# Kernel tuning notes

Measured on AMD Instinct MI355X. Metric: run time of the kernel, lower is better.

## Reference

```python
import jax, jax.numpy as jnp
import numpy as np

B, S, J, D = 8, 512, 25, 64      # batch, seq_len, n_joints, d_model
H, DH = 8, 32                    # n_heads, d_head
IN, OUT = J * D, J * DH * H      # 1600, 6400


def setup_inputs() -> dict:
    key = jax.random.key(0)
    ks = jax.random.split(key, 5)
    sc_in = 1.0 / np.sqrt(IN)
    sc_hd = 1.0 / np.sqrt(DH * H)
    return {
        "x": jax.random.normal(ks[0], (B, S, J, D), dtype=jnp.float32),
        # weights stored [in, out] (transpose of torch Linear.weight)
        "Wq": jax.random.normal(ks[1], (IN, OUT), dtype=jnp.float32) * sc_in,
        "Wk": jax.random.normal(ks[2], (IN, OUT), dtype=jnp.float32) * sc_in,
        "Wv": jax.random.normal(ks[3], (IN, OUT), dtype=jnp.float32) * sc_in,
        "Wb": jax.random.normal(ks[4], (DH * H, D), dtype=jnp.float32) * sc_hd,
    }


def reference(x, Wq, Wk, Wv, Wb):
    b, s, j, d = x.shape
    xf = x.reshape(b, s, j * d)                      # [B,S,J*D]
    q = xf @ Wq                                      # [B,S,OUT]
    k = xf @ Wk
    v = xf @ Wv
    # single fused attention over the full J*d_head*H width, scaled by d_model
    scores = jnp.einsum("bse,bte->bst", q, k) * (d ** -0.5)  # [B,S,S]
    causal = jnp.triu(jnp.ones((s, s), dtype=bool), k=1)
    scores = jnp.where(causal[None], -jnp.inf, scores)
    attn = jax.nn.softmax(scores, axis=-1)           # [B,S,S]
    ctx = jnp.einsum("bst,bte->bse", attn, v)        # [B,S,OUT]
    ctx = ctx.reshape(b, s, j, DH * H)               # [B,S,J,dh*H]
    out = ctx @ Wb                                   # [B,S,J,D]  (dropout = eval identity)
    return out
```

## Files before the change

### kernel.cpp

```cpp
#include <hip/hip_runtime.h>

typedef float  f32x4  __attribute__((ext_vector_type(4)));
typedef __bf16 bf16x8 __attribute__((ext_vector_type(8)));
typedef __bf16 bf16x4 __attribute__((ext_vector_type(4)));

__device__ __forceinline__ void gl_lds16(const void* g, void* l) {
    __builtin_amdgcn_global_load_lds(
        (const __attribute__((address_space(1))) void*)g,
        (__attribute__((address_space(3))) void*)l, 16, 0, 0);
}

__device__ __forceinline__ int xcd_swz(int wg, int nwg) {
    int xcd = wg & 7, idx = wg >> 3;
    int q = nwg >> 3, r = nwg & 7;
    return (xcd < r ? xcd * (q + 1) : r * (q + 1) + (xcd - r) * q) + idx;
}

__global__ void split_f32(const float* __restrict__ in, __bf16* __restrict__ hi,
                          __bf16* __restrict__ lo, long n) {
    long i = ((long)blockIdx.x * blockDim.x + threadIdx.x) * 4;
    if (i >= n) return;
    float4 v = *(const float4*)&in[i];
    bf16x4 h, l;
    h[0] = (__bf16)v.x; l[0] = (__bf16)(v.x - (float)h[0]);
    h[1] = (__bf16)v.y; l[1] = (__bf16)(v.y - (float)h[1]);
    h[2] = (__bf16)v.z; l[2] = (__bf16)(v.z - (float)h[2]);
    h[3] = (__bf16)v.w; l[3] = (__bf16)(v.w - (float)h[3]);
    *(bf16x4*)&hi[i] = h;
    *(bf16x4*)&lo[i] = l;
}

__global__ void copy_f32(const float* __restrict__ in, float* __restrict__ out) {
    long i = ((long)blockIdx.x * blockDim.x + threadIdx.x) * 4;
    *(float4*)&out[i] = *(const float4*)&in[i];
}

__global__ void cvt_wb(const float* __restrict__ Wb, __bf16* __restrict__ Wbt) {
    int idx = blockIdx.x * 256 + threadIdx.x;
    int k = idx >> 6, n = idx & 63;
    Wbt[n * 256 + k] = (__bf16)Wb[idx];
}

__global__ __launch_bounds__(256) void wvb_kernel(const float* __restrict__ Wv,
                                                  const __bf16* __restrict__ Wbt,
                                                  __bf16* __restrict__ WvbT) {
    const int kb = blockIdx.x;
    const int j  = blockIdx.y;
    const int tid = threadIdx.x;
    const int w = tid >> 6, l = tid & 63;
    const long r0 = (long)kb * 64 + w * 16;
    const int lr = l & 15, lk8 = (l >> 4) * 8;
    f32x4 acc[4];
    #pragma unroll
    for (int n = 0; n < 4; ++n) acc[n] = (f32x4){0.f, 0.f, 0.f, 0.f};
    #pragma unroll
    for (int kt = 0; kt < 8; ++kt) {
        const int k = kt * 32 + lk8;
        const float* ap = &Wv[(r0 + lr) * 6400 + j * 256 + k];
        float4 f0 = *(const float4*)ap;
        float4 f1 = *(const float4*)(ap + 4);
        bf16x8 a = {(__bf16)f0.x, (__bf16)f0.y, (__bf16)f0.z, (__bf16)f0.w,
                    (__bf16)f1.x, (__bf16)f1.y, (__bf16)f1.z, (__bf16)f1.w};
        #pragma unroll
        for (int n = 0; n < 4; ++n) {
            bf16x8 b = *(const bf16x8*)&Wbt[(n * 16 + lr) * 256 + k];
            acc[n] = __builtin_amdgcn_mfma_f32_16x16x32_bf16(a, b, acc[n], 0, 0, 0);
        }
    }
    const int rr = (l >> 4) * 4;
    #pragma unroll
    for (int n = 0; n < 4; ++n)
        #pragma unroll
        for (int r = 0; r < 4; ++r)
            WvbT[(long)(j * 64 + n * 16 + lr) * 1600 + r0 + rr + r] = (__bf16)acc[n][r];
}

template <int OUTMODE, bool CAUSAL, bool SWZ>
__global__ __launch_bounds__(256) void gemm3f(
    const __bf16* __restrict__ Ahi, const __bf16* __restrict__ Alo,
    const __bf16* __restrict__ Bhi, const __bf16* __restrict__ Blo,
    float* __restrict__ C, __bf16* __restrict__ Ch, __bf16* __restrict__ Cl,
    int ktot, int nkc, int lda, int ldb, int ldc, int M, int N,
    long sA, long sB, long sC, float scale)
{
    __shared__ __bf16 AsH[8192], AsL[8192], BsH[8192], BsL[8192];
    int bx = blockIdx.x, by = blockIdx.y;
    if (SWZ) {
        int f = xcd_swz(by * gridDim.x + bx, gridDim.x * gridDim.y);
        bx = f % gridDim.x; by = f / gridDim.x;
    }
    const int n0 = bx * 128, m0 = by * 128;
    if (CAUSAL && n0 > m0) return;
    const int bz = blockIdx.z;
    const int batch = bz / nkc, kc = bz % nkc;
    Ahi += (long)batch * sA; Alo += (long)batch * sA;
    Bhi += (long)batch * sB; Blo += (long)batch * sB;
    const int kbeg = (kc * ktot) / nkc;
    const int kend = ((kc + 1) * ktot) / nkc;

    const int tid = threadIdx.x;
    const int w = tid >> 6, l = tid & 63;
    const int wr = w >> 1, wc = w & 1;
    const int lr = l & 15;
    const int lk8 = (l >> 4) * 8;
    const int kswz = (lr & 7) << 3;
    const int srow = l >> 3;
    const int scol = ((l & 7) ^ (l >> 3)) * 8;

    f32x4 acc[4][4];
    #pragma unroll
    for (int m = 0; m < 4; ++m)
        #pragma unroll
        for (int n = 0; n < 4; ++n) acc[m][n] = (f32x4){0.f, 0.f, 0.f, 0.f};

    for (int kt = kbeg; kt < kend; ++kt) {
        const int k0 = kt << 6;
        __syncthreads();
        #pragma unroll
        for (int it = 0; it < 4; ++it) {
            const int j = it * 4 + w;
            const int grow = j * 8 + srow;
            const long ga = (long)(m0 + grow) * lda + k0 + scol;
            const long gb = (long)(n0 + grow) * ldb + k0 + scol;
            gl_lds16(Ahi + ga, &AsH[j * 512]);
            gl_lds16(Alo + ga, &AsL[j * 512]);
            gl_lds16(Bhi + gb, &BsH[j * 512]);
            gl_lds16(Blo + gb, &BsL[j * 512]);
        }
        __syncthreads();
        #pragma unroll
        for (int kk = 0; kk < 2; ++kk) {
            const int kx = (kk * 32 + lk8) ^ kswz;
            bf16x8 ah[4], bh[4], tt[4];
            #pragma unroll
            for (int m = 0; m < 4; ++m)
                ah[m] = *(const bf16x8*)&AsH[(wr * 64 + m * 16 + lr) * 64 + kx];
            #pragma unroll
            for (int n = 0; n < 4; ++n)
                bh[n] = *(const bf16x8*)&BsH[(wc * 64 + n * 16 + lr) * 64 + kx];
            #pragma unroll
            for (int m = 0; m < 4; ++m)
                #pragma unroll
                for (int n = 0; n < 4; ++n)
                    acc[m][n] = __builtin_amdgcn_mfma_f32_16x16x32_bf16(ah[m], bh[n], acc[m][n], 0, 0, 0);
            #pragma unroll
            for (int n = 0; n < 4; ++n)
                tt[n] = *(const bf16x8*)&BsL[(wc * 64 + n * 16 + lr) * 64 + kx];
            #pragma unroll
            for (int m = 0; m < 4; ++m)
                #pragma unroll
                for (int n = 0; n < 4; ++n)
                    acc[m][n] = __builtin_amdgcn_mfma_f32_16x16x32_bf16(ah[m], tt[n], acc[m][n], 0, 0, 0);
            #pragma unroll
            for (int m = 0; m < 4; ++m)
                tt[m] = *(const bf16x8*)&AsL[(wr * 64 + m * 16 + lr) * 64 + kx];
            #pragma unroll
            for (int m = 0; m < 4; ++m)
                #pragma unroll
                for (int n = 0; n < 4; ++n)
                    acc[m][n] = __builtin_amdgcn_mfma_f32_16x16x32_bf16(tt[m], bh[n], acc[m][n], 0, 0, 0);
        }
    }

    const int r0 = wr * 64 + (l >> 4) * 4;
    const int c0 = wc * 64 + lr;
    #pragma unroll
    for (int m = 0; m < 4; ++m)
        #pragma unroll
        for (int n = 0; n < 4; ++n)
            #pragma unroll
            for (int r = 0; r < 4; ++r) {
                int row = m0 + r0 + m * 16 + r;
                int col = n0 + c0 + n * 16;
                if (row < M && col < N) {
                    float v = acc[m][n][r] * scale;
                    long idx = (long)batch * sC + (long)row * ldc + col;
                    if (OUTMODE == 1) {
                        unsafeAtomicAdd(&C[idx], v);
                    } else if (OUTMODE == 2) {
                        __bf16 h = (__bf16)v;
                        Ch[idx] = h;
                        Cl[idx] = (__bf16)(v - (float)h);
                    } else {
                        C[idx] = v;
                    }
                }
            }
}

template <typename CT, bool TRANSC, bool SWZ>
__global__ __launch_bounds__(256) void gemm_bt(const __bf16* __restrict__ A,
                                               const __bf16* __restrict__ Bt,
                                               CT* __restrict__ C,
                                               int K, int lda, int ldb, int ldc,
                                               long sA, long sB, long sC,
                                               float scale, int causal, int Nlim) {
    __shared__ __bf16 As[8192];
    __shared__ __bf16 Bs[8192];
    int bx = blockIdx.x, by = blockIdx.y;
    if (SWZ) {
        int f = xcd_swz(by * gridDim.x + bx, gridDim.x * gridDim.y);
        bx = f % gridDim.x; by = f / gridDim.x;
    }
    const int n0 = bx * 128, m0 = by * 128;
    A  += (long)blockIdx.z * sA;
    Bt += (long)blockIdx.z * sB;
    int ksteps = K >> 6;
    if (causal == 2) { int lim = (m0 >> 6) + 2; if (lim < ksteps) ksteps = lim; }

    const int tid = threadIdx.x;
    const int w = tid >> 6, l = tid & 63;
    const int wr = w >> 1, wc = w & 1;
    const int lr = l & 15;
    const int lk8 = (l >> 4) * 8;
    const int kswz = (lr & 7) << 3;
    const int srow = l >> 3;
    const int scol = ((l & 7) ^ (l >> 3)) * 8;

    f32x4 acc[4][4];
    #pragma unroll
    for (int m = 0; m < 4; ++m)
        #pragma unroll
        for (int n = 0; n < 4; ++n) acc[m][n] = (f32x4){0.f, 0.f, 0.f, 0.f};

    for (int kt = 0; kt < ksteps; ++kt) {
        const int k0 = kt << 6;
        __syncthreads();
        #pragma unroll
        for (int it = 0; it < 4; ++it) {
            const int j = it * 4 + w;
            const int grow = j * 8 + srow;
            gl_lds16(A  + (long)(m0 + grow) * lda + k0 + scol, &As[j * 512]);
            gl_lds16(Bt + (long)(n0 + grow) * ldb + k0 + scol, &Bs[j * 512]);
        }
        __syncthreads();
        #pragma unroll
        for (int kk = 0; kk < 2; ++kk) {
            const int kx = (kk * 32 + lk8) ^ kswz;
            bf16x8 a[4], b[4];
            #pragma unroll
            for (int m = 0; m < 4; ++m)
                a[m] = *(const bf16x8*)&As[(wr * 64 + m * 16 + lr) * 64 + kx];
            #pragma unroll
            for (int n = 0; n < 4; ++n)
                b[n] = *(const bf16x8*)&Bs[(wc * 64 + n * 16 + lr) * 64 + kx];
            #pragma unroll
            for (int m = 0; m < 4; ++m)
                #pragma unroll
                for (int n = 0; n < 4; ++n)
                    acc[m][n] = __builtin_amdgcn_mfma_f32_16x16x32_bf16(a[m], b[n], acc[m][n], 0, 0, 0);
        }
    }

    const int r0 = m0 + wr * 64 + (l >> 4) * 4;
    const int c0 = n0 + wc * 64 + lr;
    #pragma unroll
    for (int m = 0; m < 4; ++m)
        #pragma unroll
        for (int n = 0; n < 4; ++n)
            #pragma unroll
            for (int r = 0; r < 4; ++r) {
                float v = acc[m][n][r] * scale;
                int row = r0 + m * 16 + r;
                int col = c0 + n * 16;
                if (TRANSC) {
                    C[(long)(row >> 9) * sC + (long)col * ldc + (row & 511)] = (CT)v;
                } else if (col < Nlim) {
                    C[(long)blockIdx.z * sC + (long)row * ldc + col] = (CT)v;
                }
            }
}

__global__ __launch_bounds__(256) void softmax_causal(const float* __restrict__ S,
                                                      __bf16* __restrict__ P) {
    __shared__ float red[8];
    const long rid = blockIdx.x;
    const int s = (int)(rid & 511);
    const float* row = S + rid * 512;
    __bf16* prow = P + rid * 512;
    const int t = threadIdx.x;
    float x0 = (t       <= s) ? row[t]       : -3.0e38f;
    float x1 = (t + 256 <= s) ? row[t + 256] : -3.0e38f;
    float m = fmaxf(x0, x1);
    #pragma unroll
    for (int off = 1; off < 64; off <<= 1) m = fmaxf(m, __shfl_xor(m, off));
    const int w = t >> 6;
    if ((t & 63) == 0) red[w] = m;
    __syncthreads();
    m = fmaxf(fmaxf(red[0], red[1]), fmaxf(red[2], red[3]));
    float e0 = __expf(x0 - m), e1 = __expf(x1 - m);
    float sum = e0 + e1;
    #pragma unroll
    for (int off = 1; off < 64; off <<= 1) sum += __shfl_xor(sum, off);
    if ((t & 63) == 0) red[4 + w] = sum;
    __syncthreads();
    sum = red[4] + red[5] + red[6] + red[7];
    const float rinv = 1.0f / sum;
    prow[t]       = (__bf16)(e0 * rinv);
    prow[t + 256] = (__bf16)(e1 * rinv);
}

extern "C" void kernel_launch(void* const* d_in, const int* in_sizes, int n_in,
                              void* d_out, int out_size, void* d_ws, size_t ws_size,
                              hipStream_t stream) {
    (void)in_sizes; (void)n_in; (void)out_size; (void)ws_size;
    const float* x  = (const float*)d_in[0];
    const float* Wq = (const float*)d_in[1];
    const float* Wk = (const float*)d_in[2];
    const float* Wv = (const float*)d_in[3];
    const float* Wb = (const float*)d_in[4];
    float* out = (float*)d_out;
    char* ws = (char*)d_ws;

    __bf16* Wqh = (__bf16*)(ws + 0);
    __bf16* Wql = (__bf16*)(ws + 20480000);
    __bf16* Wkh = (__bf16*)(ws + 40960000);
    __bf16* Wkl = (__bf16*)(ws + 61440000);
    float*  Gt  = (float*) (ws + 81920000);
    __bf16* Gth = (__bf16*)(ws + 92160000);
    __bf16* Gtl = (__bf16*)(ws + 97484800);
    __bf16* Wbt = (__bf16*)(ws + 102809600);
    __bf16* xh  = (__bf16*)(ws + 0);
    __bf16* xl  = (__bf16*)(ws + 13107200);
    __bf16* th  = (__bf16*)(ws + 26214400);
    __bf16* tl  = (__bf16*)(ws + 39321600);
    float*  s   = (float*) (ws + 81920000);
    __bf16* P   = (__bf16*)(ws + 90308608);
    __bf16* WvbT = (__bf16*)(ws + 39321600);
    __bf16* VWt  = (__bf16*)(ws + 44646400);
    float*  CtxF = (float*) (ws + 0);

    split_f32<<<10000, 256, 0, stream>>>(Wq, Wqh, Wql, 10240000L);
    split_f32<<<10000, 256, 0, stream>>>(Wk, Wkh, Wkl, 10240000L);
    hipMemsetAsync(Gt, 0, 10240000, stream);
    gemm3f<1, false, true><<<dim3(13, 13, 3), 256, 0, stream>>>(
        Wkh, Wkl, Wqh, Wql, Gt, nullptr, nullptr,
        100, 3, 6400, 6400, 1600, 1600, 1600, 0L, 0L, 0L, 1.0f);
    hipMemsetAsync((char*)Gth + 5120000, 0, 204800, stream);
    hipMemsetAsync((char*)Gtl + 5120000, 0, 204800, stream);
    split_f32<<<2500, 256, 0, stream>>>(Gt, Gth, Gtl, 2560000L);

    split_f32<<<6400, 256, 0, stream>>>(x, xh, xl, 6553600L);
    gemm3f<2, false, true><<<dim3(13, 32, 1), 256, 0, stream>>>(
        xh, xl, Gth, Gtl, nullptr, th, tl,
        25, 1, 1600, 1600, 1600, 4096, 1600, 0L, 0L, 0L, 1.0f);

    hipMemsetAsync(s, 0, 8388608, stream);
    gemm3f<1, true, false><<<dim3(4, 4, 40), 256, 0, stream>>>(
        th, tl, xh, xl, s, nullptr, nullptr,
        25, 5, 1600, 1600, 512, 512, 512, 819200L, 819200L, 262144L, 0.125f);

    softmax_causal<<<4096, 256, 0, stream>>>(s, P);

    cvt_wb<<<64, 256, 0, stream>>>(Wb, Wbt);
    hipMemsetAsync(WvbT, 0, 5324800, stream);
    wvb_kernel<<<dim3(25, 25), 256, 0, stream>>>(Wv, Wbt, WvbT);

    gemm_bt<__bf16, true, true><<<dim3(13, 32), 256, 0, stream>>>(
        xh, WvbT, VWt, 1600, 1600, 1600, 512, 0L, 0L, 851968L, 1.0f, 0, 1664);

    gemm_bt<float, false, false><<<dim3(13, 4, 8), 256, 0, stream>>>(
        P, VWt, CtxF, 512, 512, 512, 1600,
        262144L, 851968L, 819200L, 1.0f, 2, 1600);

    copy_f32<<<6400, 256, 0, stream>>>(CtxF, out);
}
```

Before: 355.4 us.

## Add 256x256-tile split-bf16 GEMM kernel for Gram and projection GEMMs

Adds gemm3v, a 512-thread kernel computing 256x256 output tiles with double-buffered LDS loads via global_load_lds. It walks the three hi/lo bf16 product terms as one flattened k-loop instead of separate passes. The Wk·Wq Gram GEMM and the x·G projection now use it with split-K atomics. The projection writes fp32 into a zeroed buffer and then runs an extra split pass into hi/lo bf16. This trades higher reuse per tile and fewer blocks for extra memset, atomic and split traffic, and edge tiles are partly wasted on the 1600-wide dimension.

```diff
diff --git a/kernel.cpp b/kernel.cpp
--- a/kernel.cpp
+++ b/kernel.cpp
@@ -73,6 +73,108 @@
         #pragma unroll
         for (int r = 0; r < 4; ++r)
             WvbT[(long)(j * 64 + n * 16 + lr) * 1600 + r0 + rr + r] = (__bf16)acc[n][r];
+}
+
+template <int OUTMODE, bool SWZ>
+__global__ __launch_bounds__(512, 2) void gemm3v(
+    const __bf16* __restrict__ Ahi, const __bf16* __restrict__ Alo,
+    const __bf16* __restrict__ Bhi, const __bf16* __restrict__ Blo,
+    float* __restrict__ C,
+    int ktot, int nkc, int lda, int ldb, int ldc, int M, int N, float scale)
+{
+    __shared__ __bf16 lds[2 * 32768];
+    int bx = blockIdx.x, by = blockIdx.y;
+    if (SWZ) {
+        int f = xcd_swz(by * gridDim.x + bx, gridDim.x * gridDim.y);
+        bx = f % gridDim.x; by = f / gridDim.x;
+    }
+    const int n0 = bx * 256, m0 = by * 256;
+    const int kc = blockIdx.z;
+    const int kbeg = (kc * ktot) / nkc;
+    const int L = ((kc + 1) * ktot) / nkc - kbeg;
+    const int KV = 3 * L;
+
+    const int tid = threadIdx.x;
+    const int w = tid >> 6, l = tid & 63;
+    const int wm = w >> 2, wn = w & 3;
+    const int lr = l & 15;
+    const int lk8 = (l >> 4) * 8;
+    const int kswz = (lr & 7) << 3;
+    const int srow = l >> 3;
+    const int scol = ((l & 7) ^ (l >> 3)) * 8;
+
+    f32x4 acc[8][4];
+    #pragma unroll
+    for (int mf = 0; mf < 8; ++mf)
+        #pragma unroll
+        for (int nf = 0; nf < 4; ++nf) acc[mf][nf] = (f32x4){0.f, 0.f, 0.f, 0.f};
+
+    auto STAGE = [&](int kv, int b) {
+        const int seg = (kv >= L) + (kv >= 2 * L);
+        const __bf16* As_ = (seg < 2) ? Ahi : Alo;
+        const __bf16* Bs_ = (seg == 1) ? Blo : Bhi;
+        const int k0 = (kbeg + kv - seg * L) << 6;
+        __bf16* base = lds + b * 32768;
+        #pragma unroll
+        for (int it = 0; it < 4; ++it) {
+            const int j = it * 8 + w;
+            const int grow = j * 8 + srow;
+            gl_lds16(As_ + (long)(m0 + grow) * lda + k0 + scol, base + j * 512);
+            gl_lds16(Bs_ + (long)(n0 + grow) * ldb + k0 + scol, base + 16384 + j * 512);
+        }
+    };
+
+    STAGE(0, 0);
+    for (int kv = 0; kv < KV; ++kv) {
+        const int cur = kv & 1;
+        if (kv + 1 < KV) {
+            STAGE(kv + 1, cur ^ 1);
+            asm volatile("s_waitcnt vmcnt(8)" ::: "memory");
+        } else {
+            asm volatile("s_waitcnt vmcnt(0)" ::: "memory");
+        }
+        __builtin_amdgcn_sched_barrier(0);
+        __builtin_amdgcn_s_barrier();
+        const __bf16* At = lds + cur * 32768;
+        const __bf16* Bt = At + 16384;
+        __builtin_amdgcn_s_setprio(1);
+        #pragma unroll
+        for (int kk = 0; kk < 2; ++kk) {
+            const int kx = (kk * 32 + lk8) ^ kswz;
+            bf16x8 a[8], b[4];
+            #pragma unroll
+            for (int mf = 0; mf < 8; ++mf)
+                a[mf] = *(const bf16x8*)&At[(wm * 128 + mf * 16 + lr) * 64 + kx];
+            #pragma unroll
+            for (int nf = 0; nf < 4; ++nf)
+                b[nf] = *(const bf16x8*)&Bt[(wn * 64 + nf * 16 + lr) * 64 + kx];
+            #pragma unroll
+            for (int mf = 0; mf < 8; ++mf)
+                #pragma unroll
+                for (int nf = 0; nf < 4; ++nf)
+                    acc[mf][nf] = __builtin_amdgcn_mfma_f32_16x16x32_bf16(a[mf], b[nf], acc[mf][nf], 0, 0, 0);
+        }
+        __builtin_amdgcn_s_setprio(0);
+        __builtin_amdgcn_sched_barrier(0);
+        __builtin_amdgcn_s_barrier();
+    }
+
+    const int rbase = m0 + wm * 128 + (l >> 4) * 4;
+    const int cbase = n0 + wn * 64 + lr;
+    #pragma unroll
+    for (int mf = 0; mf < 8; ++mf)
+        #pragma unroll
+        for (int nf = 0; nf < 4; ++nf)
+            #pragma unroll
+            for (int r = 0; r < 4; ++r) {
+                int row = rbase + mf * 16 + r;
+                int col = cbase + nf * 16;
+                if (row < M && col < N) {
+                    float v = acc[mf][nf][r] * scale;
+                    if (OUTMODE == 1) unsafeAtomicAdd(&C[(long)row * ldc + col], v);
+                    else              C[(long)row * ldc + col] = v;
+                }
+            }
 }
 
 template <int OUTMODE, bool CAUSAL, bool SWZ>
@@ -324,6 +426,7 @@
     __bf16* xl  = (__bf16*)(ws + 13107200);
     __bf16* th  = (__bf16*)(ws + 26214400);
     __bf16* tl  = (__bf16*)(ws + 39321600);
+    float*  tF  = (float*) (ws + 52428800);
     float*  s   = (float*) (ws + 81920000);
     __bf16* P   = (__bf16*)(ws + 90308608);
     __bf16* WvbT = (__bf16*)(ws + 39321600);
@@ -333,17 +436,19 @@
     split_f32<<<10000, 256, 0, stream>>>(Wq, Wqh, Wql, 10240000L);
     split_f32<<<10000, 256, 0, stream>>>(Wk, Wkh, Wkl, 10240000L);
     hipMemsetAsync(Gt, 0, 10240000, stream);
-    gemm3f<1, false, true><<<dim3(13, 13, 3), 256, 0, stream>>>(
-        Wkh, Wkl, Wqh, Wql, Gt, nullptr, nullptr,
-        100, 3, 6400, 6400, 1600, 1600, 1600, 0L, 0L, 0L, 1.0f);
+    gemm3v<1, true><<<dim3(7, 7, 5), 512, 0, stream>>>(
+        Wkh, Wkl, Wqh, Wql, Gt,
+        100, 5, 6400, 6400, 1600, 1600, 1600, 1.0f);
     hipMemsetAsync((char*)Gth + 5120000, 0, 204800, stream);
     hipMemsetAsync((char*)Gtl + 5120000, 0, 204800, stream);
     split_f32<<<2500, 256, 0, stream>>>(Gt, Gth, Gtl, 2560000L);
 
     split_f32<<<6400, 256, 0, stream>>>(x, xh, xl, 6553600L);
-    gemm3f<2, false, true><<<dim3(13, 32, 1), 256, 0, stream>>>(
-        xh, xl, Gth, Gtl, nullptr, th, tl,
-        25, 1, 1600, 1600, 1600, 4096, 1600, 0L, 0L, 0L, 1.0f);
+    hipMemsetAsync(tF, 0, 26214400, stream);
+    gemm3v<1, true><<<dim3(7, 16, 2), 512, 0, stream>>>(
+        xh, xl, Gth, Gtl, tF,
+        25, 2, 1600, 1600, 1600, 4096, 1600, 1.0f);
+    split_f32<<<6400, 256, 0, stream>>>(tF, th, tl, 6553600L);
 
     hipMemsetAsync(s, 0, 8388608, stream);
     gemm3f<1, true, false><<<dim3(4, 4, 40), 256, 0, stream>>>(
```

Result: slower. 452.6 us (+27.4%).
